# Performance work log

Hardware: AMD Instinct MI355X
Metric: run time of the kernel (lower is better)

The kernel has to match this reference:

```python
import jax, jax.numpy as jnp
import numpy as np

B, S, Hd, NH, FF = 4, 2048, 1024, 16, 4096
D = Hd // NH  # head size 64
EPS = 1e-12


def _ln(x, g, b):
    mu = jnp.mean(x, axis=-1, keepdims=True)
    var = jnp.mean(jnp.square(x - mu), axis=-1, keepdims=True)
    return (x - mu) * jax.lax.rsqrt(var + EPS) * g + b


def _rope(q, k):
    # q,k: [B,NH,S,D]; RoFormer interleaved rotary
    inv = 1.0 / (10000.0 ** (jnp.arange(0, D, 2, dtype=jnp.float32) / D))
    freqs = jnp.arange(S, dtype=jnp.float32)[:, None] * inv[None, :]  # [S,D/2]
    cos = jnp.repeat(jnp.cos(freqs), 2, axis=-1)  # [S,D]
    sin = jnp.repeat(jnp.sin(freqs), 2, axis=-1)

    def rot(x):  # [x0,x1,x2,x3,...] -> [-x1,x0,-x3,x2,...]
        return jnp.stack([-x[..., 1::2], x[..., 0::2]], axis=-1).reshape(x.shape)

    return q * cos + rot(q) * sin, k * cos + rot(k) * sin


def setup_inputs() -> dict:
    key = jax.random.key(0)
    ks = jax.random.split(key, 12)
    s = 0.02
    return {
        "x": jax.random.normal(ks[0], (B, S, Hd), jnp.float32),
        "Wq": jax.random.normal(ks[1], (Hd, Hd), jnp.float32) * s,
        "bq": jnp.zeros((Hd,), jnp.float32),
        "Wk": jax.random.normal(ks[2], (Hd, Hd), jnp.float32) * s,
        "bk": jnp.zeros((Hd,), jnp.float32),
        "Wv": jax.random.normal(ks[3], (Hd, Hd), jnp.float32) * s,
        "bv": jnp.zeros((Hd,), jnp.float32),
        "Wo": jax.random.normal(ks[4], (Hd, Hd), jnp.float32) * s,
        "bo": jnp.zeros((Hd,), jnp.float32),
        "g1": jnp.ones((Hd,), jnp.float32),
        "beta1": jnp.zeros((Hd,), jnp.float32),
        "W1": jax.random.normal(ks[5], (Hd, FF), jnp.float32) * s,
        "b1": jnp.zeros((FF,), jnp.float32),
        "W2": jax.random.normal(ks[6], (FF, Hd), jnp.float32) * s,
        "b2": jnp.zeros((Hd,), jnp.float32),
        "g2": jnp.ones((Hd,), jnp.float32),
        "beta2": jnp.zeros((Hd,), jnp.float32),
    }


def reference(x, Wq, bq, Wk, bk, Wv, bv, Wo, bo, g1, beta1, W1, b1, W2, b2, g2, beta2):
    def proj(W, b):  # [B,S,Hd] -> [B,NH,S,D]
        return (x @ W + b).reshape(B, S, NH, D).transpose(0, 2, 1, 3)

    q, k, v = proj(Wq, bq), proj(Wk, bk), proj(Wv, bv)
    q, k = _rope(q, k)
    scores = jnp.einsum('bhqd,bhkd->bhqk', q, k) / jnp.sqrt(jnp.float32(D))
    attn = jax.nn.softmax(scores, axis=-1)
    ctx = jnp.einsum('bhqk,bhkd->bhqd', attn, v)
    ctx = ctx.transpose(0, 2, 1, 3).reshape(B, S, Hd)
    attn_out = ctx @ Wo + bo
    h = _ln(x + attn_out, g1, beta1)
    ffn = jax.nn.gelu(h @ W1 + b1) @ W2 + b2
    return _ln(h + ffn, g2, beta2)
```

## Files before the change

kernel.cpp:

```cpp
#include <hip/hip_runtime.h>

#define BB   4
#define SS   2048
#define HD   1024
#define NHH  16
#define DD   64
#define FFF  4096
#define BS   (BB*SS)
#define BHN  (BB*NHH)

typedef __attribute__((ext_vector_type(8))) short v8s;
typedef __attribute__((ext_vector_type(4))) short v4s;
typedef __attribute__((ext_vector_type(4))) float v4f;

__device__ __forceinline__ short f2bf(float f) {
    union { float f; unsigned u; } v; v.f = f;
    unsigned r = (v.u + 0x7fffu + ((v.u >> 16) & 1u)) >> 16;
    return (short)r;
}
__device__ __forceinline__ float bf2f(short s) {
    union { unsigned u; float f; } v; v.u = ((unsigned)(unsigned short)s) << 16;
    return v.f;
}
__device__ __forceinline__ unsigned pktrunc(float lo, float hi) {
    return __builtin_amdgcn_perm(__builtin_bit_cast(unsigned, hi),
                                 __builtin_bit_cast(unsigned, lo), 0x07060302u);
}
__device__ __forceinline__ v4f mfma16(v8s a, v8s b, v4f c) {
    return __builtin_amdgcn_mfma_f32_16x16x32_bf16(a, b, c, 0, 0, 0);
}
__device__ __forceinline__ void cp16(void* lds, const void* g) {
    __builtin_amdgcn_global_load_lds(
        (const __attribute__((address_space(1))) unsigned*)g,
        (__attribute__((address_space(3))) unsigned*)lds, 16, 0, 0);
}


__global__ __launch_bounds__(256) void cast_bf16(const float* __restrict__ X,
                                                 short* __restrict__ Y, int n) {
    const int i = (blockIdx.x * 256 + threadIdx.x) * 4;
    if (i < n) {
        const float4 v = *(const float4*)(X + i);
        v4s o = { f2bf(v.x), f2bf(v.y), f2bf(v.z), f2bf(v.w) };
        *(v4s*)(Y + i) = o;
    }
}

__global__ __launch_bounds__(256) void rope_tab(float* __restrict__ C, float* __restrict__ Sn) {
    const int i = blockIdx.x * 256 + threadIdx.x;
    const int s = i >> 5, di = i & 31;
    const float inv = powf(10000.f, -(float)(2 * di) * (1.f / 64.f));
    const float a = (float)s * inv;
    C[i]  = cosf(a);
    Sn[i] = sinf(a);
}

__global__ __launch_bounds__(256) void transW(const float* __restrict__ W,
                                              short* __restrict__ WT, int K, int N) {
    __shared__ float T[64][65];
    const int t = threadIdx.x;
    const int r0 = blockIdx.y * 64, c0 = blockIdx.x * 64;
#pragma unroll
    for (int i = 0; i < 4; i++) {
        const int lin = t + 256 * i;
        const int r = lin >> 4, c = (lin & 15) * 4;
        const float4 v = *(const float4*)(W + (size_t)(r0 + r) * N + c0 + c);
        T[r][c] = v.x; T[r][c+1] = v.y; T[r][c+2] = v.z; T[r][c+3] = v.w;
    }
    __syncthreads();
#pragma unroll
    for (int i = 0; i < 4; i++) {
        const int lin = t + 256 * i;
        const int n = lin >> 4, k = (lin & 15) * 4;
        v4s o = { f2bf(T[k][n]), f2bf(T[k+1][n]), f2bf(T[k+2][n]), f2bf(T[k+3][n]) };
        *(v4s*)(WT + (size_t)(c0 + n) * K + r0 + k) = o;
    }
}


template <int EPI>
__global__ __launch_bounds__(256, 2) void gemm128(
    const short* __restrict__ A, const short* __restrict__ Bt,
    const float* __restrict__ bias, const float* __restrict__ bias2,
    const float* __restrict__ bias3, void* __restrict__ out,
    void* __restrict__ out2, const void* __restrict__ resid,
    const float* __restrict__ ropeC, const float* __restrict__ ropeS,
    int M, int N, int K, float oscale)
{
    __shared__ short As[128 * 64];
    __shared__ short Bs[128 * 64];
    const int t = threadIdx.x;
    const int wave = t >> 6, lane = t & 63;
    const int quad = lane >> 4, l16 = lane & 15;
    const int wm = wave & 1, wn = wave >> 1;
    const int m0 = blockIdx.x * 128, n0 = blockIdx.y * 128;

    v4f acc[4][4];
#pragma unroll
    for (int i = 0; i < 4; i++)
#pragma unroll
        for (int j = 0; j < 4; j++) { v4f z = {0.f, 0.f, 0.f, 0.f}; acc[i][j] = z; }

    const int r8 = lane >> 3;
    const int g8 = (lane & 7) ^ r8;
    const short* Asrc = A  + (size_t)(m0 + wave * 32 + r8) * K + g8 * 8;
    const short* Bsrc = Bt + (size_t)(n0 + wave * 32 + r8) * K + g8 * 8;
    short* Adst = As + wave * 2048;
    short* Bdst = Bs + wave * 2048;
    const int xsw = l16 & 7;

    for (int k0 = 0; k0 < K; k0 += 64) {
        __syncthreads();
#pragma unroll
        for (int s = 0; s < 4; s++) {
            cp16(Adst + s * 512, Asrc + (size_t)(s * 8) * K + k0);
            cp16(Bdst + s * 512, Bsrc + (size_t)(s * 8) * K + k0);
        }
        __syncthreads();
#pragma unroll
        for (int ks = 0; ks < 2; ks++) {
            v8s af[4], bfr[4];
#pragma unroll
            for (int i = 0; i < 4; i++)
                af[i] = *(const v8s*)(As + (wm * 64 + i * 16 + l16) * 64
                                         + ((ks * 4 + quad) ^ xsw) * 8);
#pragma unroll
            for (int j = 0; j < 4; j++)
                bfr[j] = *(const v8s*)(Bs + (wn * 64 + j * 16 + l16) * 64
                                          + ((ks * 4 + quad) ^ xsw) * 8);
#pragma unroll
            for (int i = 0; i < 4; i++)
#pragma unroll
                for (int j = 0; j < 4; j++)
                    acc[i][j] = mfma16(af[i], bfr[j], acc[i][j]);
        }
    }

#pragma unroll
    for (int j = 0; j < 4; j++) {
        const int col = n0 + wn * 64 + j * 16 + l16;
        if constexpr (EPI == 0) {
            const int h = col >> 10;
            const float* bp = (h == 0) ? bias : ((h == 1) ? bias2 : bias3);
            const float bval = bp[col & 1023];
            const int d = col & 63;
            const int hh = (col >> 6) & 15;
            if (h == 2) {
#pragma unroll
                for (int i = 0; i < 4; i++) {
                    const int row0 = m0 + wm * 64 + i * 16 + quad * 4;
                    const int b_ = row0 >> 11, s0 = row0 & (SS - 1);
                    v4s ov = { f2bf(acc[i][j][0] + bval), f2bf(acc[i][j][1] + bval),
                               f2bf(acc[i][j][2] + bval), f2bf(acc[i][j][3] + bval) };
                    *(v4s*)((short*)out2 + ((size_t)(b_ * NHH + hh) * DD + d) * SS + s0) = ov;
                }
            } else {
#pragma unroll
                for (int i = 0; i < 4; i++) {
#pragma unroll
                    for (int r = 0; r < 4; r++) {
                        const int row = m0 + wm * 64 + i * 16 + quad * 4 + r;
                        float v = acc[i][j][r] + bval;
                        if (h == 0) v *= oscale;
                        const int s = row & (SS - 1);
                        const float cv = ropeC[s * 32 + (d >> 1)];
                        const float sv = ropeS[s * 32 + (d >> 1)];
                        const float partner = __shfl_xor(v, 1);
                        const float o = (d & 1) ? fmaf(v, cv, partner * sv)
                                                : fmaf(v, cv, -partner * sv);
                        const int b_ = row >> 11;
                        ((short*)out)[(size_t)h * (BHN * SS * DD)
                                      + (((size_t)(b_ * NHH + hh)) * SS + s) * DD + d] = f2bf(o);
                    }
                }
            }
        } else if constexpr (EPI == 3) {
            const float bval = bias[col];
#pragma unroll
            for (int i = 0; i < 4; i++) {
#pragma unroll
                for (int r = 0; r < 4; r++) {
                    const int row = m0 + wm * 64 + i * 16 + quad * 4 + r;
                    float v = acc[i][j][r] + bval;
                    const float tq = v * v;
                    const float u = v * fmaf(0.035677408136f, tq, 0.7978845608028654f);
                    const float e = __builtin_amdgcn_exp2f(-2.8853900817779268f * u);
                    const float g = v * __builtin_amdgcn_rcpf(1.f + e);
                    ((short*)out)[(size_t)row * N + col] = f2bf(g);
                }
            }
        } else {
            const float bval = bias[col];
#pragma unroll
            for (int i = 0; i < 4; i++) {
#pragma unroll
                for (int r = 0; r < 4; r++) {
                    const int row = m0 + wm * 64 + i * 16 + quad * 4 + r;
                    float v = acc[i][j][r] + bval;
                    if constexpr (EPI == 2) v += ((const float*)resid)[(size_t)row * N + col];
                    else                    v += bf2f(((const short*)resid)[(size_t)row * N + col]);
                    ((float*)out)[(size_t)row * N + col] = v;
                }
            }
        }
    }
}

__global__ __launch_bounds__(256, 4) void attn_kernel(
    const short* __restrict__ Qh, const short* __restrict__ Kh,
    const short* __restrict__ Vt, short* __restrict__ ctx)
{
    __shared__ short Ks[64 * 64];
    __shared__ short Vs[64 * 64];
    __shared__ short Ps[4][16 * 88];
    __shared__ float Li[4][32];
    const int bh = blockIdx.x, q0 = blockIdx.y * 128;
    const int t = threadIdx.x, wave = t >> 6, lane = t & 63;
    const int quad = lane >> 4, l16 = lane & 15;

    const short* qp = Qh + ((size_t)bh * SS + q0 + wave * 32 + l16) * DD;
    v8s bq[2][2];
    bq[0][0] = *(const v8s*)(qp + quad * 8);
    bq[0][1] = *(const v8s*)(qp + 32 + quad * 8);
    bq[1][0] = *(const v8s*)(qp + (size_t)16 * DD + quad * 8);
    bq[1][1] = *(const v8s*)(qp + (size_t)16 * DD + 32 + quad * 8);

    v4f o[2][4];
#pragma unroll
    for (int qs = 0; qs < 2; qs++)
#pragma unroll
        for (int c = 0; c < 4; c++) { v4f z = {0.f, 0.f, 0.f, 0.f}; o[qs][c] = z; }
    float li[2] = {0.f, 0.f};

    const short* Kb = Kh + (size_t)bh * SS * DD;
    const short* Vb = Vt + (size_t)bh * DD * SS;
    const int r8 = lane >> 3;
    const int g8 = (lane & 7) ^ (r8 & 7);
    short* Psw = (short*)Ps[wave];
    const int xsw = l16 & 7;

    for (int kt = 0; kt < SS; kt += 64) {
        __syncthreads();
        cp16(Ks + wave * 1024,       Kb + (size_t)(kt + wave * 16 + r8) * DD + g8 * 8);
        cp16(Ks + wave * 1024 + 512, Kb + (size_t)(kt + wave * 16 + 8 + r8) * DD + g8 * 8);
        cp16(Vs + wave * 1024,       Vb + (size_t)(wave * 16 + r8) * SS + kt + g8 * 8);
        cp16(Vs + wave * 1024 + 512, Vb + (size_t)(wave * 16 + 8 + r8) * SS + kt + g8 * 8);
        __syncthreads();

        v4f sc[2][4];
#pragma unroll
        for (int c = 0; c < 4; c++) {
            const v8s k0f = *(const v8s*)(Ks + (c * 16 + l16) * 64 + ((quad    ) ^ xsw) * 8);
            const v8s k1f = *(const v8s*)(Ks + (c * 16 + l16) * 64 + ((quad + 4) ^ xsw) * 8);
#pragma unroll
            for (int qs = 0; qs < 2; qs++) {
                v4f z = {0.f, 0.f, 0.f, 0.f};
                z = mfma16(k0f, bq[qs][0], z);
                z = mfma16(k1f, bq[qs][1], z);
                sc[qs][c] = z;
            }
        }

        v8s pa[2][2];
#pragma unroll
        for (int qs = 0; qs < 2; qs++) {
            float lp = 0.f;
#pragma unroll
            for (int c = 0; c < 4; c++) {
#pragma unroll
                for (int r = 0; r < 4; r++) {
                    const float p = __builtin_amdgcn_exp2f(sc[qs][c][r]);
                    sc[qs][c][r] = p;
                    lp += p;
                }
            }
            li[qs] += lp;
            short* pw = Psw + l16 * 88;
#pragma unroll
            for (int c = 0; c < 4; c++) {
                uint2 w;
                w.x = pktrunc(sc[qs][c][0], sc[qs][c][1]);
                w.y = pktrunc(sc[qs][c][2], sc[qs][c][3]);
                *(uint2*)(pw + c * 16 + quad * 4) = w;
            }
            pa[qs][0] = *(const v8s*)(Psw + l16 * 88 + quad * 8);
            pa[qs][1] = *(const v8s*)(Psw + l16 * 88 + 32 + quad * 8);
        }

#pragma unroll
        for (int c = 0; c < 4; c++) {
            const v8s v0f = *(const v8s*)(Vs + (c * 16 + l16) * 64 + ((quad    ) ^ xsw) * 8);
            const v8s v1f = *(const v8s*)(Vs + (c * 16 + l16) * 64 + ((quad + 4) ^ xsw) * 8);
#pragma unroll
            for (int qs = 0; qs < 2; qs++) {
                o[qs][c] = mfma16(pa[qs][0], v0f, o[qs][c]);
                o[qs][c] = mfma16(pa[qs][1], v1f, o[qs][c]);
            }
        }
    }

    float linv[2][4];
#pragma unroll
    for (int qs = 0; qs < 2; qs++) {
        float lf = li[qs];
        lf += __shfl_xor(lf, 16);
        lf += __shfl_xor(lf, 32);
        if (quad == 0) Li[wave][qs * 16 + l16] = lf;
    }
    __syncthreads();
#pragma unroll
    for (int qs = 0; qs < 2; qs++) {
        const v4f lv = *(const v4f*)(&Li[wave][qs * 16 + quad * 4]);
#pragma unroll
        for (int r = 0; r < 4; r++) linv[qs][r] = __builtin_amdgcn_rcpf(lv[r]);
    }
    const int b_ = bh >> 4, h_ = bh & 15;
#pragma unroll
    for (int qs = 0; qs < 2; qs++)
#pragma unroll
        for (int c = 0; c < 4; c++)
#pragma unroll
            for (int r = 0; r < 4; r++) {
                const int s = q0 + wave * 32 + qs * 16 + quad * 4 + r;
                const int d = c * 16 + l16;
                ctx[((size_t)(b_ * SS + s)) * HD + h_ * DD + d] =
                    f2bf(o[qs][c][r] * linv[qs][r]);
            }
}

__global__ __launch_bounds__(256) void ln_kernel(
    const float* __restrict__ X, const float* __restrict__ g, const float* __restrict__ b,
    float* __restrict__ Y, short* __restrict__ Yb)
{
    const int row = blockIdx.x;
    const int t = threadIdx.x;
    const float4 v = *(const float4*)(X + (size_t)row * HD + t * 4);
    float s = v.x + v.y + v.z + v.w;
    float sq = v.x * v.x + v.y * v.y + v.z * v.z + v.w * v.w;
#pragma unroll
    for (int m = 1; m < 64; m <<= 1) { s += __shfl_xor(s, m); sq += __shfl_xor(sq, m); }
    __shared__ float red[8];
    const int wave = t >> 6, lane = t & 63;
    if (lane == 0) { red[wave] = s; red[4 + wave] = sq; }
    __syncthreads();
    s  = red[0] + red[1] + red[2] + red[3];
    sq = red[4] + red[5] + red[6] + red[7];
    const float mu = s * (1.f / HD);
    const float var = sq * (1.f / HD) - mu * mu;
    const float rs = rsqrtf(var + 1e-12f);
    const float4 gg = *(const float4*)(g + t * 4);
    const float4 bb = *(const float4*)(b + t * 4);
    const float y0 = (v.x - mu) * rs * gg.x + bb.x;
    const float y1 = (v.y - mu) * rs * gg.y + bb.y;
    const float y2 = (v.z - mu) * rs * gg.z + bb.z;
    const float y3 = (v.w - mu) * rs * gg.w + bb.w;
    if (Y)  { float4 o = { y0, y1, y2, y3 }; *(float4*)(Y + (size_t)row * HD + t * 4) = o; }
    if (Yb) { v4s o = { f2bf(y0), f2bf(y1), f2bf(y2), f2bf(y3) };
              *(v4s*)(Yb + (size_t)row * HD + t * 4) = o; }
}

extern "C" void kernel_launch(void* const* d_in, const int* in_sizes, int n_in,
                              void* d_out, int out_size, void* d_ws, size_t ws_size,
                              hipStream_t stream)
{
    (void)in_sizes; (void)n_in; (void)out_size;
    const float* x   = (const float*)d_in[0];
    const float* Wq  = (const float*)d_in[1];
    const float* bq  = (const float*)d_in[2];
    const float* Wk  = (const float*)d_in[3];
    const float* bk  = (const float*)d_in[4];
    const float* Wv  = (const float*)d_in[5];
    const float* bv  = (const float*)d_in[6];
    const float* Wo  = (const float*)d_in[7];
    const float* bo  = (const float*)d_in[8];
    const float* g1  = (const float*)d_in[9];
    const float* be1 = (const float*)d_in[10];
    const float* W1  = (const float*)d_in[11];
    const float* b1  = (const float*)d_in[12];
    const float* W2  = (const float*)d_in[13];
    const float* b2  = (const float*)d_in[14];
    const float* g2  = (const float*)d_in[15];
    const float* be2 = (const float*)d_in[16];

    char* ws = (char*)d_ws;
    size_t off = 0;
    auto alloc = [&](size_t sz) { char* p = ws + off; off += sz; return p; };
    short* xb    = (short*)alloc((size_t)BS * HD * 2);
    short* WqkvT = (short*)alloc((size_t)3 * HD * HD * 2);
    short* WoT   = (short*)alloc((size_t)HD * HD * 2);
    short* W1T   = (short*)alloc((size_t)FFF * HD * 2);
    short* W2T   = (short*)alloc((size_t)HD * FFF * 2);
    float* ropeC = (float*)alloc((size_t)SS * 32 * 4);
    float* ropeS = (float*)alloc((size_t)SS * 32 * 4);
    short* Qh    = (short*)alloc((size_t)BHN * SS * DD * 2);
    short* Kh    = (short*)alloc((size_t)BHN * SS * DD * 2);
    short* Vt    = (short*)alloc((size_t)BHN * SS * DD * 2);
    short* ctx   = (short*)alloc((size_t)BS * HD * 2);
    float* ao    = (float*)alloc((size_t)BS * HD * 4);
    if (off > ws_size) return;
    short* f1 = Qh;
    short* hb = xb;
    float* f2 = (float*)d_out;

    const float qsc = 0.125f * 1.4426950408889634f;

    cast_bf16<<<BS * HD / 1024, 256, 0, stream>>>(x, xb, BS * HD);
    rope_tab<<<SS * 32 / 256, 256, 0, stream>>>(ropeC, ropeS);
    transW<<<dim3(16, 16), 256, 0, stream>>>(Wq, WqkvT, HD, HD);
    transW<<<dim3(16, 16), 256, 0, stream>>>(Wk, WqkvT + (size_t)HD * HD, HD, HD);
    transW<<<dim3(16, 16), 256, 0, stream>>>(Wv, WqkvT + (size_t)2 * HD * HD, HD, HD);
    transW<<<dim3(16, 16), 256, 0, stream>>>(Wo, WoT, HD, HD);
    transW<<<dim3(64, 16), 256, 0, stream>>>(W1, W1T, HD, FFF);
    transW<<<dim3(16, 64), 256, 0, stream>>>(W2, W2T, FFF, HD);

    gemm128<0><<<dim3(64, 24), 256, 0, stream>>>(xb, WqkvT, bq, bk, bv, Qh, Vt,
                                                 nullptr, ropeC, ropeS, BS, 3 * HD, HD, qsc);
    attn_kernel<<<dim3(64, SS / 128), 256, 0, stream>>>(Qh, Kh, Vt, ctx);
    gemm128<2><<<dim3(64, 8), 256, 0, stream>>>(ctx, WoT, bo, nullptr, nullptr, ao,
                                                nullptr, x, nullptr, nullptr, BS, HD, HD, 1.0f);
    ln_kernel<<<BS, 256, 0, stream>>>(ao, g1, be1, nullptr, hb);
    gemm128<3><<<dim3(64, 32), 256, 0, stream>>>(hb, W1T, b1, nullptr, nullptr, f1,
                                                 nullptr, nullptr, nullptr, nullptr, BS, FFF, HD, 1.0f);
    gemm128<4><<<dim3(64, 8), 256, 0, stream>>>(f1, W2T, b2, nullptr, nullptr, f2,
                                                nullptr, hb, nullptr, nullptr, BS, HD, FFF, 1.0f);
    ln_kernel<<<BS, 256, 0, stream>>>(f2, g2, be2, (float*)d_out, nullptr);
}
```

Measured before the change: 505.1 us.

## Double-buffer LDS tiles in GEMM and attention, fuse weight transposes

```diff
diff --git a/kernel.cpp b/kernel.cpp
--- a/kernel.cpp
+++ b/kernel.cpp
@@ -55,11 +55,33 @@
     Sn[i] = sinf(a);
 }
 
-__global__ __launch_bounds__(256) void transW(const float* __restrict__ W,
-                                              short* __restrict__ WT, int K, int N) {
+__global__ __launch_bounds__(256) void transW_all(
+    const float* __restrict__ Wq, const float* __restrict__ Wk,
+    const float* __restrict__ Wv, const float* __restrict__ Wo,
+    const float* __restrict__ W1, const float* __restrict__ W2,
+    short* __restrict__ WqkvT, short* __restrict__ WoT,
+    short* __restrict__ W1T, short* __restrict__ W2T)
+{
+    const int id = blockIdx.x;
+    const float* W; short* WT; int K, N, bx, by;
+    if (id < 768) {
+        const int m = id >> 8;
+        W = (m == 0) ? Wq : (m == 1) ? Wk : Wv;
+        WT = WqkvT + (size_t)m * HD * HD;
+        K = HD; N = HD; const int r = id & 255; bx = r & 15; by = r >> 4;
+    } else if (id < 1024) {
+        W = Wo; WT = WoT; K = HD; N = HD;
+        const int r = id - 768; bx = r & 15; by = r >> 4;
+    } else if (id < 2048) {
+        W = W1; WT = W1T; K = HD; N = FFF;
+        const int r = id - 1024; bx = r & 63; by = r >> 6;
+    } else {
+        W = W2; WT = W2T; K = FFF; N = HD;
+        const int r = id - 2048; bx = r & 15; by = r >> 4;
+    }
     __shared__ float T[64][65];
     const int t = threadIdx.x;
-    const int r0 = blockIdx.y * 64, c0 = blockIdx.x * 64;
+    const int r0 = by * 64, c0 = bx * 64;
 #pragma unroll
     for (int i = 0; i < 4; i++) {
         const int lin = t + 256 * i;
@@ -87,8 +109,8 @@
     const float* __restrict__ ropeC, const float* __restrict__ ropeS,
     int M, int N, int K, float oscale)
 {
-    __shared__ short As[128 * 64];
-    __shared__ short Bs[128 * 64];
+    __shared__ short As[2][128 * 64];
+    __shared__ short Bs[2][128 * 64];
     const int t = threadIdx.x;
     const int wave = t >> 6, lane = t & 63;
     const int quad = lane >> 4, l16 = lane & 15;
@@ -105,35 +127,42 @@
     const int g8 = (lane & 7) ^ r8;
     const short* Asrc = A  + (size_t)(m0 + wave * 32 + r8) * K + g8 * 8;
     const short* Bsrc = Bt + (size_t)(n0 + wave * 32 + r8) * K + g8 * 8;
-    short* Adst = As + wave * 2048;
-    short* Bdst = Bs + wave * 2048;
+    const int wofs = wave * 2048;
     const int xsw = l16 & 7;
 
+    auto stage = [&](int buf, int kofs) {
+#pragma unroll
+        for (int s = 0; s < 4; s++) {
+            cp16(&As[buf][wofs + s * 512], Asrc + (size_t)(s * 8) * K + kofs);
+            cp16(&Bs[buf][wofs + s * 512], Bsrc + (size_t)(s * 8) * K + kofs);
+        }
+    };
+
+    stage(0, 0);
+    __syncthreads();
+
+    int cur = 0;
     for (int k0 = 0; k0 < K; k0 += 64) {
-        __syncthreads();
-#pragma unroll
-        for (int s = 0; s < 4; s++) {
-            cp16(Adst + s * 512, Asrc + (size_t)(s * 8) * K + k0);
-            cp16(Bdst + s * 512, Bsrc + (size_t)(s * 8) * K + k0);
-        }
-        __syncthreads();
+        if (k0 + 64 < K) stage(cur ^ 1, k0 + 64);
 #pragma unroll
         for (int ks = 0; ks < 2; ks++) {
             v8s af[4], bfr[4];
 #pragma unroll
             for (int i = 0; i < 4; i++)
-                af[i] = *(const v8s*)(As + (wm * 64 + i * 16 + l16) * 64
-                                         + ((ks * 4 + quad) ^ xsw) * 8);
+                af[i] = *(const v8s*)(&As[cur][(wm * 64 + i * 16 + l16) * 64
+                                              + ((ks * 4 + quad) ^ xsw) * 8]);
 #pragma unroll
             for (int j = 0; j < 4; j++)
-                bfr[j] = *(const v8s*)(Bs + (wn * 64 + j * 16 + l16) * 64
-                                          + ((ks * 4 + quad) ^ xsw) * 8);
+                bfr[j] = *(const v8s*)(&Bs[cur][(wn * 64 + j * 16 + l16) * 64
+                                               + ((ks * 4 + quad) ^ xsw) * 8]);
 #pragma unroll
             for (int i = 0; i < 4; i++)
 #pragma unroll
                 for (int j = 0; j < 4; j++)
                     acc[i][j] = mfma16(af[i], bfr[j], acc[i][j]);
         }
+        __syncthreads();
+        cur ^= 1;
     }
 
 #pragma unroll
@@ -206,12 +235,12 @@
     }
 }
 
-__global__ __launch_bounds__(256, 4) void attn_kernel(
+__global__ __launch_bounds__(256, 3) void attn_kernel(
     const short* __restrict__ Qh, const short* __restrict__ Kh,
     const short* __restrict__ Vt, short* __restrict__ ctx)
 {
-    __shared__ short Ks[64 * 64];
-    __shared__ short Vs[64 * 64];
+    __shared__ short Ks[2][64 * 64];
+    __shared__ short Vs[2][64 * 64];
     __shared__ short Ps[4][16 * 88];
     __shared__ float Li[4][32];
     const int bh = blockIdx.x, q0 = blockIdx.y * 128;
@@ -239,19 +268,25 @@
     short* Psw = (short*)Ps[wave];
     const int xsw = l16 & 7;
 
+    auto stage = [&](int buf, int kt) {
+        cp16(&Ks[buf][wave * 1024],       Kb + (size_t)(kt + wave * 16 + r8) * DD + g8 * 8);
+        cp16(&Ks[buf][wave * 1024 + 512], Kb + (size_t)(kt + wave * 16 + 8 + r8) * DD + g8 * 8);
+        cp16(&Vs[buf][wave * 1024],       Vb + (size_t)(wave * 16 + r8) * SS + kt + g8 * 8);
+        cp16(&Vs[buf][wave * 1024 + 512], Vb + (size_t)(wave * 16 + 8 + r8) * SS + kt + g8 * 8);
+    };
+
+    stage(0, 0);
+    __syncthreads();
+
+    int cur = 0;
     for (int kt = 0; kt < SS; kt += 64) {
-        __syncthreads();
-        cp16(Ks + wave * 1024,       Kb + (size_t)(kt + wave * 16 + r8) * DD + g8 * 8);
-        cp16(Ks + wave * 1024 + 512, Kb + (size_t)(kt + wave * 16 + 8 + r8) * DD + g8 * 8);
-        cp16(Vs + wave * 1024,       Vb + (size_t)(wave * 16 + r8) * SS + kt + g8 * 8);
-        cp16(Vs + wave * 1024 + 512, Vb + (size_t)(wave * 16 + 8 + r8) * SS + kt + g8 * 8);
-        __syncthreads();
+        if (kt + 64 < SS) stage(cur ^ 1, kt + 64);
 
         v4f sc[2][4];
 #pragma unroll
         for (int c = 0; c < 4; c++) {
-            const v8s k0f = *(const v8s*)(Ks + (c * 16 + l16) * 64 + ((quad    ) ^ xsw) * 8);
-            const v8s k1f = *(const v8s*)(Ks + (c * 16 + l16) * 64 + ((quad + 4) ^ xsw) * 8);
+            const v8s k0f = *(const v8s*)(&Ks[cur][(c * 16 + l16) * 64 + ((quad    ) ^ xsw) * 8]);
+            const v8s k1f = *(const v8s*)(&Ks[cur][(c * 16 + l16) * 64 + ((quad + 4) ^ xsw) * 8]);
 #pragma unroll
             for (int qs = 0; qs < 2; qs++) {
                 v4f z = {0.f, 0.f, 0.f, 0.f};
@@ -289,14 +324,17 @@
 
 #pragma unroll
         for (int c = 0; c < 4; c++) {
-            const v8s v0f = *(const v8s*)(Vs + (c * 16 + l16) * 64 + ((quad    ) ^ xsw) * 8);
-            const v8s v1f = *(const v8s*)(Vs + (c * 16 + l16) * 64 + ((quad + 4) ^ xsw) * 8);
+            const v8s v0f = *(const v8s*)(&Vs[cur][(c * 16 + l16) * 64 + ((quad    ) ^ xsw) * 8]);
+            const v8s v1f = *(const v8s*)(&Vs[cur][(c * 16 + l16) * 64 + ((quad + 4) ^ xsw) * 8]);
 #pragma unroll
             for (int qs = 0; qs < 2; qs++) {
                 o[qs][c] = mfma16(pa[qs][0], v0f, o[qs][c]);
                 o[qs][c] = mfma16(pa[qs][1], v1f, o[qs][c]);
             }
         }
+
+        __syncthreads();
+        cur ^= 1;
     }
 
     float linv[2][4];
@@ -406,12 +444,8 @@
 
     cast_bf16<<<BS * HD / 1024, 256, 0, stream>>>(x, xb, BS * HD);
     rope_tab<<<SS * 32 / 256, 256, 0, stream>>>(ropeC, ropeS);
-    transW<<<dim3(16, 16), 256, 0, stream>>>(Wq, WqkvT, HD, HD);
-    transW<<<dim3(16, 16), 256, 0, stream>>>(Wk, WqkvT + (size_t)HD * HD, HD, HD);
-    transW<<<dim3(16, 16), 256, 0, stream>>>(Wv, WqkvT + (size_t)2 * HD * HD, HD, HD);
-    transW<<<dim3(16, 16), 256, 0, stream>>>(Wo, WoT, HD, HD);
-    transW<<<dim3(64, 16), 256, 0, stream>>>(W1, W1T, HD, FFF);
-    transW<<<dim3(16, 64), 256, 0, stream>>>(W2, W2T, FFF, HD);
+    transW_all<<<3072, 256, 0, stream>>>(Wq, Wk, Wv, Wo, W1, W2,
+                                         WqkvT, WoT, W1T, W2T);
 
     gemm128<0><<<dim3(64, 24), 256, 0, stream>>>(xb, WqkvT, bq, bk, bv, Qh, Vt,
                                                  nullptr, ropeC, ropeS, BS, 3 * HD, HD, qsc);
```

After: 509.6 us. About the same (+0.9%).
